# Performance work log

Measured on AMD Instinct MI355X. Metric: run time of the kernel, lower is better.

The kernel has to match this reference:

```python
import jax, jax.numpy as jnp
import numpy as np

N_NODES = 100000
N_EDGES = 3200000
K_STEPS = 10
ALPHA = 0.1


def setup_inputs() -> dict:
    key = jax.random.key(0)
    k = jax.random.split(key, 6)
    x = jax.random.normal(k[0], (N_NODES, 512), dtype=jnp.float32)
    W1 = jax.random.normal(k[1], (256, 512), dtype=jnp.float32) * (1.0 / np.sqrt(512))
    b1 = jnp.zeros((256,), dtype=jnp.float32)
    W2 = jax.random.normal(k[2], (16, 256), dtype=jnp.float32) * (1.0 / np.sqrt(256))
    b2 = jnp.zeros((16,), dtype=jnp.float32)
    edge_index = jax.random.randint(k[3], (2, N_EDGES), 0, N_NODES, dtype=jnp.int64)
    return {"x": x, "W1": W1, "b1": b1, "W2": W2, "b2": b2, "edge_index": edge_index}


def reference(x, W1, b1, W2, b2, edge_index):
    N = x.shape[0]
    # MLP preamble (dropout inactive at inference)
    h = jax.nn.relu(x @ W1.T + b1) @ W2.T + b2  # [N, classes]

    # gcn_norm with self-loops: A_hat = D^-1/2 (A + I) D^-1/2
    loop = jnp.arange(N, dtype=edge_index.dtype)
    src = jnp.concatenate([edge_index[0], loop])
    dst = jnp.concatenate([edge_index[1], loop])
    deg = jax.ops.segment_sum(jnp.ones(src.shape[0], dtype=h.dtype), dst, num_segments=N)
    dinv = jnp.where(deg > 0, jax.lax.rsqrt(deg), 0.0)
    norm = dinv[src] * dinv[dst]  # [E+N]

    def step(z, _):
        msg = z[src] * norm[:, None]  # gather + scale
        agg = jax.ops.segment_sum(msg, dst, num_segments=N)  # scatter-add
        return (1.0 - ALPHA) * agg + ALPHA * h, None

    z, _ = jax.lax.scan(step, h, None, length=K_STEPS)
    return jax.nn.log_softmax(z, axis=1)
```

## Files before the change

kernel.cpp:

```cpp
#include <hip/hip_runtime.h>
#include <hip/hip_bf16.h>
#include <stdint.h>

#define N_NODES 100000
#define N_EDGES 3200000
#define ALPHA   0.1f

typedef __attribute__((ext_vector_type(8))) short v8s;
typedef __attribute__((ext_vector_type(4))) float f32x4;

__device__ __forceinline__ uint32_t bf16_rne(float f) {
    uint32_t u = __float_as_uint(f);
    return (u + 0x7FFFu + ((u >> 16) & 1u)) >> 16;
}
__device__ __forceinline__ float bf16_f32(uint32_t b) { return __uint_as_float(b << 16); }

__global__ __launch_bounds__(256) void w1_frag_kernel(
    const float* __restrict__ W1, uint4* __restrict__ W1f)
{
    int tid = blockIdx.x * 256 + threadIdx.x;
    int ks = tid >> 10, T = (tid >> 6) & 15, l = tid & 63;
    int row = T * 16 + (l & 15);
    int kb  = ks * 32 + (l >> 4) * 8;
    const float* src = W1 + (size_t)row * 512 + kb;
    float4 f0 = *(const float4*)(src);
    float4 f1 = *(const float4*)(src + 4);
    float f[8] = {f0.x, f0.y, f0.z, f0.w, f1.x, f1.y, f1.z, f1.w};
    uint32_t hi[8], lo[8];
#pragma unroll
    for (int j = 0; j < 8; ++j) {
        hi[j] = bf16_rne(f[j]);
        lo[j] = bf16_rne(f[j] - bf16_f32(hi[j]));
    }
    uint4 H = make_uint4(hi[0] | (hi[1] << 16), hi[2] | (hi[3] << 16),
                         hi[4] | (hi[5] << 16), hi[6] | (hi[7] << 16));
    uint4 L = make_uint4(lo[0] | (lo[1] << 16), lo[2] | (lo[3] << 16),
                         lo[4] | (lo[5] << 16), lo[6] | (lo[7] << 16));
    size_t base = ((size_t)(ks * 2) * 16 + T) * 64 + l;
    W1f[base]        = H;
    W1f[base + 1024] = L;
}

__global__ __launch_bounds__(256, 2) void mlp_kernel(
    const float* __restrict__ x, const uint4* __restrict__ W1f,
    const float* __restrict__ b1, const float* __restrict__ W2,
    const float* __restrict__ b2, const float* __restrict__ dinv,
    float* __restrict__ h, float* __restrict__ hs, int n)
{
    __shared__ __align__(16) char smem[33280];
    char*  xs   = smem;
    float* W2s  = (float*)smem;
    float* part = (float*)(smem + 16640);

    const int tid = threadIdx.x;
    const int w = tid >> 6, l = tid & 63;
    const int l15 = l & 15, q = l >> 4;
    const int row0 = blockIdx.x * 64;

    const int s_l15 = tid & 15;
    const int s_seg = (tid >> 4) & 3;
    const int s_u   = tid >> 6;
    const int s_grow = row0 + s_u * 16 + s_l15;

    f32x4 acc[4][4];
#pragma unroll
    for (int mt = 0; mt < 4; ++mt)
#pragma unroll
        for (int nt = 0; nt < 4; ++nt) acc[mt][nt] = (f32x4){0.f, 0.f, 0.f, 0.f};

    for (int ks = 0; ks < 16; ++ks) {
        uint4 aHu[4], aLu[4];
#pragma unroll
        for (int mt = 0; mt < 4; ++mt) {
            size_t cidx = ((size_t)(ks * 2) * 16 + (w * 4 + mt)) * 64 + l;
            aHu[mt] = W1f[cidx];
            aLu[mt] = W1f[cidx + 1024];
        }
        float4 f0 = make_float4(0.f, 0.f, 0.f, 0.f), f1 = f0;
        if (s_grow < n) {
            const float* xp = x + (size_t)s_grow * 512 + ks * 32 + s_seg * 8;
            f0 = *(const float4*)(xp);
            f1 = *(const float4*)(xp + 4);
        }
        float f[8] = {f0.x, f0.y, f0.z, f0.w, f1.x, f1.y, f1.z, f1.w};
        uint32_t hi[8], lo[8];
#pragma unroll
        for (int j = 0; j < 8; ++j) {
            hi[j] = bf16_rne(f[j]);
            lo[j] = bf16_rne(f[j] - bf16_f32(hi[j]));
        }
        uint4 H = make_uint4(hi[0] | (hi[1] << 16), hi[2] | (hi[3] << 16),
                             hi[4] | (hi[5] << 16), hi[6] | (hi[7] << 16));
        uint4 L = make_uint4(lo[0] | (lo[1] << 16), lo[2] | (lo[3] << 16),
                             lo[4] | (lo[5] << 16), lo[6] | (lo[7] << 16));
        __syncthreads();
        *(uint4*)(xs +        s_u * 1024 + (s_seg * 16 + s_l15) * 16) = H;
        *(uint4*)(xs + 4096 + s_u * 1024 + (s_seg * 16 + s_l15) * 16) = L;
        __syncthreads();

        v8s bH[4], bL[4];
#pragma unroll
        for (int nt = 0; nt < 4; ++nt) {
            bH[nt] = *(v8s*)(xs +        nt * 1024 + l * 16);
            bL[nt] = *(v8s*)(xs + 4096 + nt * 1024 + l * 16);
        }
#pragma unroll
        for (int mt = 0; mt < 4; ++mt) {
            v8s aH = *(v8s*)&aHu[mt];
            v8s aL = *(v8s*)&aLu[mt];
#pragma unroll
            for (int nt = 0; nt < 4; ++nt) {
                f32x4 c = acc[mt][nt];
                c = __builtin_amdgcn_mfma_f32_16x16x32_bf16(aH, bH[nt], c, 0, 0, 0);
                c = __builtin_amdgcn_mfma_f32_16x16x32_bf16(aH, bL[nt], c, 0, 0, 0);
                c = __builtin_amdgcn_mfma_f32_16x16x32_bf16(aL, bH[nt], c, 0, 0, 0);
                acc[mt][nt] = c;
            }
        }
    }

#pragma unroll
    for (int mt = 0; mt < 4; ++mt) {
        float4 bv = *(const float4*)(b1 + w * 64 + mt * 16 + q * 4);
#pragma unroll
        for (int nt = 0; nt < 4; ++nt) {
            acc[mt][nt][0] = fmaxf(acc[mt][nt][0] + bv.x, 0.f);
            acc[mt][nt][1] = fmaxf(acc[mt][nt][1] + bv.y, 0.f);
            acc[mt][nt][2] = fmaxf(acc[mt][nt][2] + bv.z, 0.f);
            acc[mt][nt][3] = fmaxf(acc[mt][nt][3] + bv.w, 0.f);
        }
    }

    __syncthreads();
    {
        int c = tid >> 4, k16 = (tid & 15) * 16;
#pragma unroll
        for (int i = 0; i < 4; ++i)
            *(float4*)(W2s + c * 260 + k16 + i * 4) =
                *(const float4*)(W2 + c * 256 + k16 + i * 4);
    }
    __syncthreads();

#pragma unroll
    for (int c4 = 0; c4 < 4; ++c4) {
        float p2[4][4];
#pragma unroll
        for (int nt = 0; nt < 4; ++nt)
#pragma unroll
            for (int cc = 0; cc < 4; ++cc) p2[nt][cc] = 0.f;
#pragma unroll
        for (int mt = 0; mt < 4; ++mt)
#pragma unroll
            for (int cc = 0; cc < 4; ++cc) {
                float4 wv = *(float4*)(W2s + (c4 * 4 + cc) * 260 + w * 64 + mt * 16 + q * 4);
#pragma unroll
                for (int nt = 0; nt < 4; ++nt)
                    p2[nt][cc] += acc[mt][nt][0] * wv.x + acc[mt][nt][1] * wv.y +
                                  acc[mt][nt][2] * wv.z + acc[mt][nt][3] * wv.w;
            }
#pragma unroll
        for (int nt = 0; nt < 4; ++nt)
#pragma unroll
            for (int cc = 0; cc < 4; ++cc) {
                p2[nt][cc] += __shfl_xor(p2[nt][cc], 16);
                p2[nt][cc] += __shfl_xor(p2[nt][cc], 32);
            }
        if (q == c4) {
#pragma unroll
            for (int nt = 0; nt < 4; ++nt)
                *(float4*)(part + ((w * 64 + nt * 16 + l15) << 4) + c4 * 4) =
                    make_float4(p2[nt][0], p2[nt][1], p2[nt][2], p2[nt][3]);
        }
    }
    __syncthreads();
    {
        int node = tid >> 2, c4 = (tid & 3) * 4;
        float4 s = make_float4(0.f, 0.f, 0.f, 0.f);
#pragma unroll
        for (int ww = 0; ww < 4; ++ww) {
            float4 v = *(float4*)(part + ((ww * 64 + node) << 4) + c4);
            s.x += v.x; s.y += v.y; s.z += v.z; s.w += v.w;
        }
        float4 bv = *(const float4*)(b2 + c4);
        int grow = row0 + node;
        if (grow < n) {
            float4 hv = make_float4(s.x + bv.x, s.y + bv.y, s.z + bv.z, s.w + bv.w);
            *(float4*)(h + (size_t)grow * 16 + c4) = hv;
            float di = dinv[grow];
            *(float4*)(hs + (size_t)grow * 16 + c4) =
                make_float4(di * hv.x, di * hv.y, di * hv.z, di * hv.w);
        }
    }
}

__global__ void hist_kernel(const int* __restrict__ dst, int* __restrict__ cnt, int e)
{
    int i = blockIdx.x * blockDim.x + threadIdx.x;
    if (i < e) atomicAdd(&cnt[dst[i]], 1);
}

__global__ void dinv_kernel(const int* __restrict__ cnt, float* __restrict__ dinv, int n)
{
    int i = blockIdx.x * blockDim.x + threadIdx.x;
    if (i < n) dinv[i] = rsqrtf((float)cnt[i] + 1.0f);
}

__global__ __launch_bounds__(256) void scan1_kernel(
    const int* __restrict__ cnt, int* __restrict__ row_loc,
    int* __restrict__ bsum, int n)
{
    __shared__ int sm[256];
    int i = blockIdx.x * 256 + threadIdx.x;
    int v = (i < n) ? cnt[i] : 0;
    sm[threadIdx.x] = v;
    __syncthreads();
#pragma unroll
    for (int off = 1; off < 256; off <<= 1) {
        int t = (threadIdx.x >= off) ? sm[threadIdx.x - off] : 0;
        __syncthreads();
        sm[threadIdx.x] += t;
        __syncthreads();
    }
    if (i < n) row_loc[i] = sm[threadIdx.x] - v;
    if (threadIdx.x == 255) bsum[blockIdx.x] = sm[255];
}

__global__ __launch_bounds__(512) void scan2_kernel(
    const int* __restrict__ bsum, int* __restrict__ boff, int nb)
{
    __shared__ int sm[512];
    int i = threadIdx.x;
    int v = (i < nb) ? bsum[i] : 0;
    sm[i] = v;
    __syncthreads();
#pragma unroll
    for (int off = 1; off < 512; off <<= 1) {
        int t = (i >= off) ? sm[i - off] : 0;
        __syncthreads();
        sm[i] += t;
        __syncthreads();
    }
    if (i < nb) boff[i] = sm[i] - v;
}

__global__ void scan3_kernel(int* __restrict__ row_st, const int* __restrict__ boff,
                             int* __restrict__ cursor, int n, int e)
{
    int i = blockIdx.x * blockDim.x + threadIdx.x;
    if (i < n) {
        int r = row_st[i] + boff[i >> 8];
        row_st[i] = r;
        cursor[i] = r;
    }
    if (i == 0) row_st[n] = e;
}

#define SC_CHUNK 2048
__global__ __launch_bounds__(256) void scatter8_kernel(
    const int* __restrict__ src, const int* __restrict__ dst,
    int* __restrict__ cursor, int* __restrict__ csr_s, int e)
{
    const int w    = blockIdx.x & 7;
    const int base = (blockIdx.x >> 3) * SC_CHUNK;
    const int wlo  = w * (N_NODES / 8);
    const int whi  = wlo + (N_NODES / 8);
#pragma unroll
    for (int t = 0; t < SC_CHUNK / 256; ++t) {
        int i = base + t * 256 + threadIdx.x;
        if (i < e) {
            int d = dst[i];
            if (d >= wlo && d < whi) {
                int s = src[i];
                int pos = atomicAdd(&cursor[d], 1);
                csr_s[pos] = s;
            }
        }
    }
}

__global__ __launch_bounds__(256) void prop_kernel(
    const int* __restrict__ csr_s, const int* __restrict__ row_st,
    const float* __restrict__ dinv, const float* __restrict__ zs_in,
    const float* __restrict__ hmat, float* __restrict__ out,
    int n, int is_last)
{
    const int d = blockIdx.x * 64 + (threadIdx.x >> 2);
    if (d >= n) return;
    const int f4 = (threadIdx.x & 3) * 4;
    const int rs = row_st[d], re = row_st[d + 1];

    float4 S = *(const float4*)(zs_in + (size_t)d * 16 + f4);

    int j = rs;
    int head = (rs + 3) & ~3;
    if (head > re) head = re;
    for (; j < head; ++j) {
        int s0 = csr_s[j];
        const float4 a = *(const float4*)(zs_in + (size_t)s0 * 16 + f4);
        S.x += a.x; S.y += a.y; S.z += a.z; S.w += a.w;
    }
    for (; j + 4 <= re; j += 4) {
        int4 sv = *(const int4*)(csr_s + j);
        const float4 a = *(const float4*)(zs_in + (size_t)sv.x * 16 + f4);
        const float4 b = *(const float4*)(zs_in + (size_t)sv.y * 16 + f4);
        const float4 c = *(const float4*)(zs_in + (size_t)sv.z * 16 + f4);
        const float4 e = *(const float4*)(zs_in + (size_t)sv.w * 16 + f4);
        S.x += (a.x + b.x) + (c.x + e.x);
        S.y += (a.y + b.y) + (c.y + e.y);
        S.z += (a.z + b.z) + (c.z + e.z);
        S.w += (a.w + b.w) + (c.w + e.w);
    }
    for (; j < re; ++j) {
        int s0 = csr_s[j];
        const float4 a = *(const float4*)(zs_in + (size_t)s0 * 16 + f4);
        S.x += a.x; S.y += a.y; S.z += a.z; S.w += a.w;
    }

    const float di = dinv[d];
    const float4 hv = *(const float4*)(hmat + (size_t)d * 16 + f4);
    float4 zn;
    zn.x = fmaf(1.0f - ALPHA, di * S.x, ALPHA * hv.x);
    zn.y = fmaf(1.0f - ALPHA, di * S.y, ALPHA * hv.y);
    zn.z = fmaf(1.0f - ALPHA, di * S.z, ALPHA * hv.z);
    zn.w = fmaf(1.0f - ALPHA, di * S.w, ALPHA * hv.w);
    if (!is_last) {
        *(float4*)(out + (size_t)d * 16 + f4) =
            make_float4(di * zn.x, di * zn.y, di * zn.z, di * zn.w);
    } else {
        float m = fmaxf(fmaxf(zn.x, zn.y), fmaxf(zn.z, zn.w));
        m = fmaxf(m, __shfl_xor(m, 1));
        m = fmaxf(m, __shfl_xor(m, 2));
        float ss = expf(zn.x - m) + expf(zn.y - m) + expf(zn.z - m) + expf(zn.w - m);
        ss += __shfl_xor(ss, 1);
        ss += __shfl_xor(ss, 2);
        float ls = logf(ss);
        *(float4*)(out + (size_t)d * 16 + f4) =
            make_float4(zn.x - m - ls, zn.y - m - ls, zn.z - m - ls, zn.w - m - ls);
    }
}

extern "C" void kernel_launch(void* const* d_in, const int* in_sizes, int n_in,
                              void* d_out, int out_size, void* d_ws, size_t ws_size,
                              hipStream_t stream)
{
    const float* x  = (const float*)d_in[0];
    const float* W1 = (const float*)d_in[1];
    const float* b1 = (const float*)d_in[2];
    const float* W2 = (const float*)d_in[3];
    const float* b2 = (const float*)d_in[4];
    const int*   ei = (const int*)d_in[5];

    const int N = N_NODES;
    const int E = N_EDGES;
    const int* srcp = ei;
    const int* dstp = ei + E;

    float* ws = (float*)d_ws;
    float* h       = ws;
    float* ZSA     = ws + 1600000;
    float* ZSB     = ws + 3200000;
    float* dinv    = ws + 4800000;
    int*   row_st  = (int*)(ws + 4900000);
    int*   csr_s   = (int*)(ws + 5000004);
    int*   cnt     = (int*)(ws);
    int*   cursor  = (int*)(ws + 100000);
    int*   bsum    = (int*)(ws + 200000);
    int*   boff    = (int*)(ws + 200512);
    uint4* W1f     = (uint4*)(ws + 1600000);

    const int NB_SCAN = (N + 255) / 256;

    hipMemsetAsync(cnt, 0, (size_t)N * sizeof(int), stream);
    hist_kernel<<<(E + 255) / 256, 256, 0, stream>>>(dstp, cnt, E);
    dinv_kernel<<<(N + 255) / 256, 256, 0, stream>>>(cnt, dinv, N);
    scan1_kernel<<<NB_SCAN, 256, 0, stream>>>(cnt, row_st, bsum, N);
    scan2_kernel<<<1, 512, 0, stream>>>(bsum, boff, NB_SCAN);
    scan3_kernel<<<(N + 255) / 256, 256, 0, stream>>>(row_st, boff, cursor, N, E);
    {
        const int nchunks = (E + SC_CHUNK - 1) / SC_CHUNK;
        scatter8_kernel<<<nchunks * 8, 256, 0, stream>>>(srcp, dstp, cursor, csr_s, E);
    }
    w1_frag_kernel<<<64, 256, 0, stream>>>(W1, W1f);
    mlp_kernel<<<(N + 63) / 64, 256, 0, stream>>>(x, W1f, b1, W2, b2, dinv, h, ZSB, N);

    const int NB_PROP = (N + 63) / 64;
    for (int k = 0; k < 10; ++k) {
        const int last = (k == 9) ? 1 : 0;
        const float* zin = (k == 0) ? ZSB : ((k & 1) ? ZSA : ZSB);
        float* zo = last ? (float*)d_out : ((k & 1) ? ZSB : ZSA);
        prop_kernel<<<NB_PROP, 256, 0, stream>>>(csr_s, row_st, dinv, zin, h, zo,
                                                 N, last);
    }
}
```

Measured before the change: 1.091 ms.

## Pad CSR rows to multiples of 16 and split each row across four sub-lanes

Each node's CSR row is padded to a multiple of 16 entries, filled with a dummy node index whose z row is zeroed, so the gather loop needs no head or tail handling and always issues aligned int4 index loads. Each destination now uses 16 threads (4 sub-groups × 4 feature quads), each sub-group covering a strided slice of the row; partial sums are combined with xor shuffles and the self-loop term is added afterwards. This aims to raise memory-level parallelism for the ~32-degree rows and remove scalar tail loops. In exchange the padded CSR holds more entries (up to 4.8M), adds a fill pass over it, and gathers extra dummy rows.

New measurement: 977.2 us. 1.12x faster.

```diff
diff --git a/kernel.cpp b/kernel.cpp
--- a/kernel.cpp
+++ b/kernel.cpp
@@ -199,19 +199,33 @@
     if (i < e) atomicAdd(&cnt[dst[i]], 1);
 }
 
-__global__ void dinv_kernel(const int* __restrict__ cnt, float* __restrict__ dinv, int n)
+__global__ void dinv_kernel(const int* __restrict__ cnt, float* __restrict__ dinv,
+                            int* __restrict__ pcnt,
+                            float* __restrict__ zsA_dummy, float* __restrict__ zsB_dummy,
+                            int n)
 {
     int i = blockIdx.x * blockDim.x + threadIdx.x;
-    if (i < n) dinv[i] = rsqrtf((float)cnt[i] + 1.0f);
+    if (i < n) {
+        int c = cnt[i];
+        dinv[i] = rsqrtf((float)c + 1.0f);
+        pcnt[i] = (c + 15) & ~15;
+    }
+    if (i < 16) { zsA_dummy[i] = 0.0f; zsB_dummy[i] = 0.0f; }
+}
+
+__global__ void fill_kernel(int4* __restrict__ p, int v, int cnt4)
+{
+    int i = blockIdx.x * blockDim.x + threadIdx.x;
+    if (i < cnt4) p[i] = make_int4(v, v, v, v);
 }
 
 __global__ __launch_bounds__(256) void scan1_kernel(
-    const int* __restrict__ cnt, int* __restrict__ row_loc,
+    const int* __restrict__ pcnt, int* __restrict__ row_loc,
     int* __restrict__ bsum, int n)
 {
     __shared__ int sm[256];
     int i = blockIdx.x * 256 + threadIdx.x;
-    int v = (i < n) ? cnt[i] : 0;
+    int v = (i < n) ? pcnt[i] : 0;
     sm[threadIdx.x] = v;
     __syncthreads();
 #pragma unroll
@@ -221,7 +235,7 @@
         sm[threadIdx.x] += t;
         __syncthreads();
     }
-    if (i < n) row_loc[i] = sm[threadIdx.x] - v;
+    if (i <= n) row_loc[i] = sm[threadIdx.x] - v;
     if (threadIdx.x == 255) bsum[blockIdx.x] = sm[255];
 }
 
@@ -244,15 +258,14 @@
 }
 
 __global__ void scan3_kernel(int* __restrict__ row_st, const int* __restrict__ boff,
-                             int* __restrict__ cursor, int n, int e)
+                             int* __restrict__ cursor, int n)
 {
     int i = blockIdx.x * blockDim.x + threadIdx.x;
-    if (i < n) {
+    if (i <= n) {
         int r = row_st[i] + boff[i >> 8];
         row_st[i] = r;
-        cursor[i] = r;
-    }
-    if (i == 0) row_st[n] = e;
+        if (i < n) cursor[i] = r;
+    }
 }
 
 #define SC_CHUNK 2048
@@ -284,37 +297,51 @@
     const float* __restrict__ hmat, float* __restrict__ out,
     int n, int is_last)
 {
-    const int d = blockIdx.x * 64 + (threadIdx.x >> 2);
+    const int t = threadIdx.x;
+    const int d = blockIdx.x * 16 + (t >> 4);
     if (d >= n) return;
-    const int f4 = (threadIdx.x & 3) * 4;
+    const int lane16 = t & 15;
+    const int sub = lane16 >> 2;
+    const int f4 = (lane16 & 3) * 4;
     const int rs = row_st[d], re = row_st[d + 1];
 
-    float4 S = *(const float4*)(zs_in + (size_t)d * 16 + f4);
-
-    int j = rs;
-    int head = (rs + 3) & ~3;
-    if (head > re) head = re;
-    for (; j < head; ++j) {
-        int s0 = csr_s[j];
-        const float4 a = *(const float4*)(zs_in + (size_t)s0 * 16 + f4);
-        S.x += a.x; S.y += a.y; S.z += a.z; S.w += a.w;
-    }
-    for (; j + 4 <= re; j += 4) {
-        int4 sv = *(const int4*)(csr_s + j);
-        const float4 a = *(const float4*)(zs_in + (size_t)sv.x * 16 + f4);
-        const float4 b = *(const float4*)(zs_in + (size_t)sv.y * 16 + f4);
-        const float4 c = *(const float4*)(zs_in + (size_t)sv.z * 16 + f4);
-        const float4 e = *(const float4*)(zs_in + (size_t)sv.w * 16 + f4);
-        S.x += (a.x + b.x) + (c.x + e.x);
-        S.y += (a.y + b.y) + (c.y + e.y);
-        S.z += (a.z + b.z) + (c.z + e.z);
-        S.w += (a.w + b.w) + (c.w + e.w);
-    }
-    for (; j < re; ++j) {
-        int s0 = csr_s[j];
-        const float4 a = *(const float4*)(zs_in + (size_t)s0 * 16 + f4);
-        S.x += a.x; S.y += a.y; S.z += a.z; S.w += a.w;
-    }
+    float4 S = make_float4(0.f, 0.f, 0.f, 0.f);
+    int j = rs + sub * 4;
+    for (; j + 16 < re; j += 32) {
+        int4 s0 = *(const int4*)(csr_s + j);
+        int4 s1 = *(const int4*)(csr_s + j + 16);
+        const float4 a0 = *(const float4*)(zs_in + (size_t)s0.x * 16 + f4);
+        const float4 b0 = *(const float4*)(zs_in + (size_t)s0.y * 16 + f4);
+        const float4 c0 = *(const float4*)(zs_in + (size_t)s0.z * 16 + f4);
+        const float4 e0 = *(const float4*)(zs_in + (size_t)s0.w * 16 + f4);
+        const float4 a1 = *(const float4*)(zs_in + (size_t)s1.x * 16 + f4);
+        const float4 b1 = *(const float4*)(zs_in + (size_t)s1.y * 16 + f4);
+        const float4 c1 = *(const float4*)(zs_in + (size_t)s1.z * 16 + f4);
+        const float4 e1 = *(const float4*)(zs_in + (size_t)s1.w * 16 + f4);
+        S.x += ((a0.x + b0.x) + (c0.x + e0.x)) + ((a1.x + b1.x) + (c1.x + e1.x));
+        S.y += ((a0.y + b0.y) + (c0.y + e0.y)) + ((a1.y + b1.y) + (c1.y + e1.y));
+        S.z += ((a0.z + b0.z) + (c0.z + e0.z)) + ((a1.z + b1.z) + (c1.z + e1.z));
+        S.w += ((a0.w + b0.w) + (c0.w + e0.w)) + ((a1.w + b1.w) + (c1.w + e1.w));
+    }
+    if (j < re) {
+        int4 s0 = *(const int4*)(csr_s + j);
+        const float4 a0 = *(const float4*)(zs_in + (size_t)s0.x * 16 + f4);
+        const float4 b0 = *(const float4*)(zs_in + (size_t)s0.y * 16 + f4);
+        const float4 c0 = *(const float4*)(zs_in + (size_t)s0.z * 16 + f4);
+        const float4 e0 = *(const float4*)(zs_in + (size_t)s0.w * 16 + f4);
+        S.x += (a0.x + b0.x) + (c0.x + e0.x);
+        S.y += (a0.y + b0.y) + (c0.y + e0.y);
+        S.z += (a0.z + b0.z) + (c0.z + e0.z);
+        S.w += (a0.w + b0.w) + (c0.w + e0.w);
+    }
+
+    S.x += __shfl_xor(S.x, 4); S.y += __shfl_xor(S.y, 4);
+    S.z += __shfl_xor(S.z, 4); S.w += __shfl_xor(S.w, 4);
+    S.x += __shfl_xor(S.x, 8); S.y += __shfl_xor(S.y, 8);
+    S.z += __shfl_xor(S.z, 8); S.w += __shfl_xor(S.w, 8);
+
+    const float4 self = *(const float4*)(zs_in + (size_t)d * 16 + f4);
+    S.x += self.x; S.y += self.y; S.z += self.z; S.w += self.w;
 
     const float di = dinv[d];
     const float4 hv = *(const float4*)(hmat + (size_t)d * 16 + f4);
@@ -324,8 +351,9 @@
     zn.z = fmaf(1.0f - ALPHA, di * S.z, ALPHA * hv.z);
     zn.w = fmaf(1.0f - ALPHA, di * S.w, ALPHA * hv.w);
     if (!is_last) {
-        *(float4*)(out + (size_t)d * 16 + f4) =
-            make_float4(di * zn.x, di * zn.y, di * zn.z, di * zn.w);
+        if (sub == 0)
+            *(float4*)(out + (size_t)d * 16 + f4) =
+                make_float4(di * zn.x, di * zn.y, di * zn.z, di * zn.w);
     } else {
         float m = fmaxf(fmaxf(zn.x, zn.y), fmaxf(zn.z, zn.w));
         m = fmaxf(m, __shfl_xor(m, 1));
@@ -334,8 +362,9 @@
         ss += __shfl_xor(ss, 1);
         ss += __shfl_xor(ss, 2);
         float ls = logf(ss);
-        *(float4*)(out + (size_t)d * 16 + f4) =
-            make_float4(zn.x - m - ls, zn.y - m - ls, zn.z - m - ls, zn.w - m - ls);
+        if (sub == 0)
+            *(float4*)(out + (size_t)d * 16 + f4) =
+                make_float4(zn.x - m - ls, zn.y - m - ls, zn.z - m - ls, zn.w - m - ls);
     }
 }
 
@@ -352,30 +381,36 @@
 
     const int N = N_NODES;
     const int E = N_EDGES;
+    const int EP_MAX = 4800000;
     const int* srcp = ei;
     const int* dstp = ei + E;
 
     float* ws = (float*)d_ws;
     float* h       = ws;
     float* ZSA     = ws + 1600000;
-    float* ZSB     = ws + 3200000;
-    float* dinv    = ws + 4800000;
-    int*   row_st  = (int*)(ws + 4900000);
-    int*   csr_s   = (int*)(ws + 5000004);
+    float* ZSB     = ws + 3200016;
+    float* dinv    = ws + 4800032;
+    int*   row_st  = (int*)(ws + 4900032);
+    int*   csr_s   = (int*)(ws + 5000036);
     int*   cnt     = (int*)(ws);
     int*   cursor  = (int*)(ws + 100000);
     int*   bsum    = (int*)(ws + 200000);
     int*   boff    = (int*)(ws + 200512);
+    int*   pcnt    = (int*)(ws + 201024);
     uint4* W1f     = (uint4*)(ws + 1600000);
+    float* zsA_dummy = ZSA + (size_t)N * 16;
+    float* zsB_dummy = ZSB + (size_t)N * 16;
 
     const int NB_SCAN = (N + 255) / 256;
 
     hipMemsetAsync(cnt, 0, (size_t)N * sizeof(int), stream);
     hist_kernel<<<(E + 255) / 256, 256, 0, stream>>>(dstp, cnt, E);
-    dinv_kernel<<<(N + 255) / 256, 256, 0, stream>>>(cnt, dinv, N);
-    scan1_kernel<<<NB_SCAN, 256, 0, stream>>>(cnt, row_st, bsum, N);
+    dinv_kernel<<<(N + 255) / 256, 256, 0, stream>>>(cnt, dinv, pcnt,
+                                                     zsA_dummy, zsB_dummy, N);
+    fill_kernel<<<(EP_MAX / 4 + 255) / 256, 256, 0, stream>>>((int4*)csr_s, N, EP_MAX / 4);
+    scan1_kernel<<<NB_SCAN, 256, 0, stream>>>(pcnt, row_st, bsum, N);
     scan2_kernel<<<1, 512, 0, stream>>>(bsum, boff, NB_SCAN);
-    scan3_kernel<<<(N + 255) / 256, 256, 0, stream>>>(row_st, boff, cursor, N, E);
+    scan3_kernel<<<(N + 256) / 256, 256, 0, stream>>>(row_st, boff, cursor, N);
     {
         const int nchunks = (E + SC_CHUNK - 1) / SC_CHUNK;
         scatter8_kernel<<<nchunks * 8, 256, 0, stream>>>(srcp, dstp, cursor, csr_s, E);
@@ -383,7 +418,7 @@
     w1_frag_kernel<<<64, 256, 0, stream>>>(W1, W1f);
     mlp_kernel<<<(N + 63) / 64, 256, 0, stream>>>(x, W1f, b1, W2, b2, dinv, h, ZSB, N);
 
-    const int NB_PROP = (N + 63) / 64;
+    const int NB_PROP = (N + 15) / 16;
     for (int k = 0; k < 10; ++k) {
         const int last = (k == 9) ? 1 : 0;
         const float* zin = (k == 0) ? ZSB : ((k & 1) ? ZSA : ZSB);
```
